# Kernel optimization log

Hardware: AMD Instinct MI355X
Metric: run time of the kernel (lower is better)

The kernel has to match this reference:

```python
import jax, jax.numpy as jnp
import numpy as np

EPS = 1e-5

def layer_norm(x, gamma, beta):
    mu = jnp.mean(x, axis=-1, keepdims=True)
    var = jnp.mean(jnp.square(x - mu), axis=-1, keepdims=True)
    return (x - mu) * jax.lax.rsqrt(var + EPS) * gamma + beta

def reverse_sigmoid(x):
    # torch version clamps value to [0.001, 0.999] with a detached offset ->
    # straight-through: clipped value, identity gradient into the logit.
    y = x + jax.lax.stop_gradient(jnp.clip(x, 0.001, 0.999) - x)
    return jnp.log(y) - jnp.log1p(-y)

def setup_inputs() -> dict:
    key = jax.random.key(0)
    ks = jax.random.split(key, 8)
    N, D, A, F8, FD = 32768, 1024, 256, 8, 64
    inp = {
        "unary_term": jax.random.normal(ks[0], (N, D), jnp.float32),
        "pair_term": jax.random.normal(ks[1], (N, D), jnp.float32),
        "auxiliary_term": jax.random.normal(ks[2], (N, A), jnp.float32),
        "auxiliary_gating_weight": jax.random.uniform(ks[3], (N,), jnp.float32),
        # self.w params: LayerNorm(2D) + Linear(2D, FD)
        "ln_gamma": jnp.ones((2 * D,), jnp.float32),
        "ln_beta": jnp.zeros((2 * D,), jnp.float32),
        "W": jax.random.normal(ks[4], (2 * D, FD), jnp.float32) * 0.02,
        "b": jnp.zeros((FD,), jnp.float32),
        # self.w_aux params: LayerNorm(A) + Linear(A, 8)
        "ln_aux_gamma": jnp.ones((A,), jnp.float32),
        "ln_aux_beta": jnp.zeros((A,), jnp.float32),
        "W_aux": jax.random.normal(ks[5], (A, F8), jnp.float32) * 0.02,
        "b_aux": jnp.zeros((F8,), jnp.float32),
        # use_auxiliary_gate_weight=True -> both init to 0.33
        "gate_weight": jnp.array(0.33, jnp.float32),
        "aux_gate_weight": jnp.array(0.33, jnp.float32),
    }
    return inp

def reference(unary_term, pair_term, auxiliary_term, auxiliary_gating_weight,
              ln_gamma, ln_beta, W, b, ln_aux_gamma, ln_aux_beta, W_aux, b_aux,
              gate_weight, aux_gate_weight):
    # paired_feats = relu(cat([unary, pair], 1))
    paired = jax.nn.relu(jnp.concatenate([unary_term, pair_term], axis=1))  # [N, 2D]
    # gate = sigmoid(Linear(relu(LN(paired))))
    gate = jax.nn.sigmoid(jax.nn.relu(layer_norm(paired, ln_gamma, ln_beta)) @ W + b)  # [N, FD]
    aux_gate = jax.nn.sigmoid(jax.nn.relu(layer_norm(auxiliary_term, ln_aux_gamma, ln_aux_beta)) @ W_aux + b_aux)  # [N, 8]
    gate = jnp.mean(gate, axis=1)        # [N]
    aux_gate = jnp.mean(aux_gate, axis=1)  # [N]
    logit = gate_weight * reverse_sigmoid(gate) + aux_gate_weight * reverse_sigmoid(aux_gate)
    g = jax.nn.sigmoid(logit) * auxiliary_gating_weight  # use_auxiliary_gate_weight=True
    output = pair_term * g[:, None]
    return (output, g)
```

## Files before the change

kernel.cpp:

```cpp
#include <hip/hip_runtime.h>
#include <math.h>


#define EPS_LN 1e-5f

typedef __attribute__((ext_vector_type(8))) short short8;
typedef __attribute__((ext_vector_type(4))) float f32x4;

__device__ __forceinline__ unsigned short f2bf(float f) {
  unsigned int u = __float_as_uint(f);
  u += 0x7FFFu + ((u >> 16) & 1u);
  return (unsigned short)(u >> 16);
}

__device__ __forceinline__ float wsum64(float v) {
  v += __shfl_xor(v, 32);
  v += __shfl_xor(v, 16);
  v += __shfl_xor(v, 8);
  v += __shfl_xor(v, 4);
  v += __shfl_xor(v, 2);
  v += __shfl_xor(v, 1);
  return v;
}

__device__ __forceinline__ float sigmoidf_(float x) {
  return 1.0f / (1.0f + __expf(-x));
}

__device__ __forceinline__ float rsigf(float x) {
  float y = fminf(fmaxf(x, 0.001f), 0.999f);
  return logf(y) - log1pf(-y);
}

__device__ __forceinline__ ushort4 norm_pack(float4 x, float4 g, float4 b,
                                             float mu, float rstd) {
  ushort4 o;
  o.x = f2bf(fmaxf((x.x - mu) * rstd * g.x + b.x, 0.f));
  o.y = f2bf(fmaxf((x.y - mu) * rstd * g.y + b.y, 0.f));
  o.z = f2bf(fmaxf((x.z - mu) * rstd * g.z + b.z, 0.f));
  o.w = f2bf(fmaxf((x.w - mu) * rstd * g.w + b.w, 0.f));
  return o;
}

__global__ void prep_wfrag(const float* __restrict__ W,
                           unsigned short* __restrict__ wfrag) {
  const int lane = threadIdx.x;
  const int b = blockIdx.x;
  const int ntile = b >> 6;
  const int kb = b & 63;
  const int f = (ntile << 4) + (lane & 15);
  const int kbase = (kb << 5) + ((lane >> 4) << 3);
  unsigned short tmp[8];
#pragma unroll
  for (int j = 0; j < 8; ++j) tmp[j] = f2bf(W[(size_t)(kbase + j) * 64 + f]);
  ushort4* dst = reinterpret_cast<ushort4*>(wfrag + (((size_t)b * 64 + lane) << 3));
  dst[0] = make_ushort4(tmp[0], tmp[1], tmp[2], tmp[3]);
  dst[1] = make_ushort4(tmp[4], tmp[5], tmp[6], tmp[7]);
}

__global__ void __launch_bounds__(256, 2) fused_main(
    const float* __restrict__ unary, const float* __restrict__ pair,
    const float* __restrict__ aux, const float* __restrict__ auxw,
    const float* __restrict__ ln_g, const float* __restrict__ ln_b,
    const float* __restrict__ b_lin,
    const float* __restrict__ ln_ag, const float* __restrict__ ln_ab,
    const float* __restrict__ W_aux, const float* __restrict__ b_aux,
    const float* __restrict__ gw, const float* __restrict__ agw,
    const unsigned short* __restrict__ wfrag,
    float* __restrict__ out, float* __restrict__ out_g) {
  __shared__ unsigned short act_lds[16 * 2048];

  const int tid = threadIdx.x;
  const int w = tid >> 6;
  const int lane = tid & 63;
  const int base = blockIdx.x << 4;

  float auxg0 = 0.f, auxg1 = 0.f, auxg2 = 0.f, auxg3 = 0.f;

#pragma unroll
  for (int i = 0; i < 4; ++i) {
    const int rl = (w << 2) + i;
    const int row = base + rl;
    const int sw = rl & 7;

    const float4* u4 = reinterpret_cast<const float4*>(unary + (size_t)row * 1024);
    const float4* p4 = reinterpret_cast<const float4*>(pair + (size_t)row * 1024);
    float4 uv[4], pv[4];
#pragma unroll
    for (int j = 0; j < 4; ++j) {
      uv[j] = u4[lane + 64 * j];
      pv[j] = p4[lane + 64 * j];
    }
    float s = 0.f, sq = 0.f;
#pragma unroll
    for (int j = 0; j < 4; ++j) {
      uv[j].x = fmaxf(uv[j].x, 0.f); uv[j].y = fmaxf(uv[j].y, 0.f);
      uv[j].z = fmaxf(uv[j].z, 0.f); uv[j].w = fmaxf(uv[j].w, 0.f);
      pv[j].x = fmaxf(pv[j].x, 0.f); pv[j].y = fmaxf(pv[j].y, 0.f);
      pv[j].z = fmaxf(pv[j].z, 0.f); pv[j].w = fmaxf(pv[j].w, 0.f);
      s += uv[j].x + uv[j].y + uv[j].z + uv[j].w;
      s += pv[j].x + pv[j].y + pv[j].z + pv[j].w;
      sq += uv[j].x * uv[j].x + uv[j].y * uv[j].y + uv[j].z * uv[j].z + uv[j].w * uv[j].w;
      sq += pv[j].x * pv[j].x + pv[j].y * pv[j].y + pv[j].z * pv[j].z + pv[j].w * pv[j].w;
    }
    s = wsum64(s);
    sq = wsum64(sq);
    const float mu = s * (1.f / 2048.f);
    const float rstd = rsqrtf(sq * (1.f / 2048.f) - mu * mu + EPS_LN);

    const float4* g4 = reinterpret_cast<const float4*>(ln_g);
    const float4* bb4 = reinterpret_cast<const float4*>(ln_b);
#pragma unroll
    for (int j = 0; j < 4; ++j) {
      const int idx = lane + 64 * j;
      const int off = (lane & 1) << 2;
      ushort4 o = norm_pack(uv[j], g4[idx], bb4[idx], mu, rstd);
      int addr = (rl << 11) + ((((idx >> 1)) ^ sw) << 3) + off;
      *reinterpret_cast<ushort4*>(&act_lds[addr]) = o;
      ushort4 o2 = norm_pack(pv[j], g4[256 + idx], bb4[256 + idx], mu, rstd);
      int addr2 = (rl << 11) + (((128 + (idx >> 1)) ^ sw) << 3) + off;
      *reinterpret_cast<ushort4*>(&act_lds[addr2]) = o2;
    }

    const float4 av = reinterpret_cast<const float4*>(aux + (size_t)row * 256)[lane];
    float as = av.x + av.y + av.z + av.w;
    float asq = av.x * av.x + av.y * av.y + av.z * av.z + av.w * av.w;
    as = wsum64(as);
    asq = wsum64(asq);
    const float amu = as * (1.f / 256.f);
    const float arstd = rsqrtf(asq * (1.f / 256.f) - amu * amu + EPS_LN);
    const float4 ag = reinterpret_cast<const float4*>(ln_ag)[lane];
    const float4 ab = reinterpret_cast<const float4*>(ln_ab)[lane];
    float aa[4];
    aa[0] = fmaxf((av.x - amu) * arstd * ag.x + ab.x, 0.f);
    aa[1] = fmaxf((av.y - amu) * arstd * ag.y + ab.y, 0.f);
    aa[2] = fmaxf((av.z - amu) * arstd * ag.z + ab.z, 0.f);
    aa[3] = fmaxf((av.w - amu) * arstd * ag.w + ab.w, 0.f);
    float pf[8];
#pragma unroll
    for (int f = 0; f < 8; ++f) pf[f] = 0.f;
#pragma unroll
    for (int t = 0; t < 4; ++t) {
      const float4* wr = reinterpret_cast<const float4*>(W_aux + (((size_t)lane << 2) + t) * 8);
      float4 wa = wr[0], wb = wr[1];
      pf[0] += aa[t] * wa.x; pf[1] += aa[t] * wa.y;
      pf[2] += aa[t] * wa.z; pf[3] += aa[t] * wa.w;
      pf[4] += aa[t] * wb.x; pf[5] += aa[t] * wb.y;
      pf[6] += aa[t] * wb.z; pf[7] += aa[t] * wb.w;
    }
    float ss = 0.f;
#pragma unroll
    for (int f = 0; f < 8; ++f) {
      float v = wsum64(pf[f]);
      ss += sigmoidf_(v + b_aux[f]);
    }
    const float agv = ss * (1.f / 8.f);
    if (i == 0) auxg0 = agv;
    else if (i == 1) auxg1 = agv;
    else if (i == 2) auxg2 = agv;
    else auxg3 = agv;
  }

  __syncthreads();

  f32x4 acc = {0.f, 0.f, 0.f, 0.f};
  const int arow = lane & 15;
  const int quad = lane >> 4;
  const int abase = arow << 11;
  const int asw = arow & 7;
  const unsigned short* wbase = wfrag + ((size_t)(w << 6) << 9);
#pragma unroll 8
  for (int kb = 0; kb < 64; ++kb) {
    const int c = (kb << 2) + quad;
    const short8 afrag =
        *reinterpret_cast<const short8*>(&act_lds[abase + ((c ^ asw) << 3)]);
    const short8 bfrag =
        *reinterpret_cast<const short8*>(wbase + ((size_t)kb << 9) + (lane << 3));
    acc = __builtin_amdgcn_mfma_f32_16x16x32_bf16(afrag, bfrag, acc, 0, 0, 0);
  }

  const float bl = b_lin[(w << 4) + arow];
  float sred[4];
#pragma unroll
  for (int i = 0; i < 4; ++i) {
    float v = sigmoidf_(acc[i] + bl);
    v += __shfl_xor(v, 1);
    v += __shfl_xor(v, 2);
    v += __shfl_xor(v, 4);
    v += __shfl_xor(v, 8);
    sred[i] = v;
  }

  __syncthreads();
  float* gate_part = reinterpret_cast<float*>(act_lds);
  if (arow == 0) {
#pragma unroll
    for (int i = 0; i < 4; ++i)
      gate_part[(w << 4) + (quad << 2) + i] = sred[i];
  }
  __syncthreads();

  const float gwt = gw[0];
  const float agwt = agw[0];
#pragma unroll
  for (int i = 0; i < 4; ++i) {
    const int rl = (w << 2) + i;
    const int row = base + rl;
    const float gsum = gate_part[rl] + gate_part[16 + rl] +
                       gate_part[32 + rl] + gate_part[48 + rl];
    const float gate = gsum * (1.f / 64.f);
    const float auxg = (i == 0) ? auxg0 : (i == 1) ? auxg1 : (i == 2) ? auxg2 : auxg3;
    const float logit = gwt * rsigf(gate) + agwt * rsigf(auxg);
    const float g = sigmoidf_(logit) * auxw[row];

    const float4* p4 = reinterpret_cast<const float4*>(pair + (size_t)row * 1024);
    float4* o4 = reinterpret_cast<float4*>(out + (size_t)row * 1024);
#pragma unroll
    for (int j = 0; j < 4; ++j) {
      float4 pv = p4[lane + 64 * j];
      pv.x *= g; pv.y *= g; pv.z *= g; pv.w *= g;
      o4[lane + 64 * j] = pv;
    }
    if (lane == 0) out_g[row] = g;
  }
}

extern "C" void kernel_launch(void* const* d_in, const int* in_sizes, int n_in,
                              void* d_out, int out_size, void* d_ws, size_t ws_size,
                              hipStream_t stream) {
  const float* unary = (const float*)d_in[0];
  const float* pair  = (const float*)d_in[1];
  const float* aux   = (const float*)d_in[2];
  const float* auxw  = (const float*)d_in[3];
  const float* ln_g  = (const float*)d_in[4];
  const float* ln_b  = (const float*)d_in[5];
  const float* W     = (const float*)d_in[6];
  const float* b     = (const float*)d_in[7];
  const float* ln_ag = (const float*)d_in[8];
  const float* ln_ab = (const float*)d_in[9];
  const float* W_aux = (const float*)d_in[10];
  const float* b_aux = (const float*)d_in[11];
  const float* gw    = (const float*)d_in[12];
  const float* agw   = (const float*)d_in[13];

  const int N = in_sizes[3];
  unsigned short* wfrag = (unsigned short*)d_ws;
  float* out = (float*)d_out;
  float* out_g = out + (size_t)N * 1024;

  prep_wfrag<<<256, 64, 0, stream>>>(W, wfrag);
  fused_main<<<N / 16, 256, 0, stream>>>(unary, pair, aux, auxw, ln_g, ln_b, b,
                                         ln_ag, ln_ab, W_aux, b_aux, gw, agw,
                                         wfrag, out, out_g);
}
```

Baseline: 480.9 us.

## Halve rows per block, raise occupancy, and move aux linear to MFMA

Each block now handles 8 rows instead of 16, which halves LDS use per block and lets launch bounds ask for 4 blocks per CU instead of 2, so more loads can be in flight on this memory-bound kernel. The auxiliary LayerNorm+Linear now writes bf16 activations to LDS and does its matmul with MFMA, using W_aux repacked by the prep kernel. This replaces the scalar FMA loop and its eight 64-lane shuffle reductions. The four LayerNorm reductions are merged into one shuffle loop. In exchange, half of each 16-row MFMA tile is wasted, and the aux path drops to bf16 precision.

```diff
diff --git a/kernel.cpp b/kernel.cpp
--- a/kernel.cpp
+++ b/kernel.cpp
@@ -11,16 +11,6 @@
   unsigned int u = __float_as_uint(f);
   u += 0x7FFFu + ((u >> 16) & 1u);
   return (unsigned short)(u >> 16);
-}
-
-__device__ __forceinline__ float wsum64(float v) {
-  v += __shfl_xor(v, 32);
-  v += __shfl_xor(v, 16);
-  v += __shfl_xor(v, 8);
-  v += __shfl_xor(v, 4);
-  v += __shfl_xor(v, 2);
-  v += __shfl_xor(v, 1);
-  return v;
 }
 
 __device__ __forceinline__ float sigmoidf_(float x) {
@@ -43,45 +33,59 @@
 }
 
 __global__ void prep_wfrag(const float* __restrict__ W,
+                           const float* __restrict__ W_aux,
                            unsigned short* __restrict__ wfrag) {
   const int lane = threadIdx.x;
   const int b = blockIdx.x;
-  const int ntile = b >> 6;
-  const int kb = b & 63;
-  const int f = (ntile << 4) + (lane & 15);
-  const int kbase = (kb << 5) + ((lane >> 4) << 3);
   unsigned short tmp[8];
-#pragma unroll
-  for (int j = 0; j < 8; ++j) tmp[j] = f2bf(W[(size_t)(kbase + j) * 64 + f]);
-  ushort4* dst = reinterpret_cast<ushort4*>(wfrag + (((size_t)b * 64 + lane) << 3));
-  dst[0] = make_ushort4(tmp[0], tmp[1], tmp[2], tmp[3]);
-  dst[1] = make_ushort4(tmp[4], tmp[5], tmp[6], tmp[7]);
-}
-
-__global__ void __launch_bounds__(256, 2) fused_main(
+  if (b < 256) {
+    const int ntile = b >> 6;
+    const int kb = b & 63;
+    const int f = (ntile << 4) + (lane & 15);
+    const int kbase = (kb << 5) + ((lane >> 4) << 3);
+#pragma unroll
+    for (int j = 0; j < 8; ++j) tmp[j] = f2bf(W[(size_t)(kbase + j) * 64 + f]);
+    ushort4* dst = reinterpret_cast<ushort4*>(wfrag + (((size_t)b * 64 + lane) << 3));
+    dst[0] = make_ushort4(tmp[0], tmp[1], tmp[2], tmp[3]);
+    dst[1] = make_ushort4(tmp[4], tmp[5], tmp[6], tmp[7]);
+  } else {
+    const int kb = b - 256;
+    const int f = lane & 15;
+    const int kbase = (kb << 5) + ((lane >> 4) << 3);
+#pragma unroll
+    for (int j = 0; j < 8; ++j)
+      tmp[j] = (f < 8) ? f2bf(W_aux[(size_t)(kbase + j) * 8 + f]) : (unsigned short)0;
+    ushort4* dst = reinterpret_cast<ushort4*>(
+        wfrag + 131072 + (((size_t)kb * 64 + lane) << 3));
+    dst[0] = make_ushort4(tmp[0], tmp[1], tmp[2], tmp[3]);
+    dst[1] = make_ushort4(tmp[4], tmp[5], tmp[6], tmp[7]);
+  }
+}
+
+__global__ void __launch_bounds__(256, 4) fused_main(
     const float* __restrict__ unary, const float* __restrict__ pair,
     const float* __restrict__ aux, const float* __restrict__ auxw,
     const float* __restrict__ ln_g, const float* __restrict__ ln_b,
     const float* __restrict__ b_lin,
     const float* __restrict__ ln_ag, const float* __restrict__ ln_ab,
-    const float* __restrict__ W_aux, const float* __restrict__ b_aux,
+    const float* __restrict__ b_aux,
     const float* __restrict__ gw, const float* __restrict__ agw,
     const unsigned short* __restrict__ wfrag,
     float* __restrict__ out, float* __restrict__ out_g) {
-  __shared__ unsigned short act_lds[16 * 2048];
+  __shared__ unsigned short act_lds[8 * 2048];
+  __shared__ unsigned short aux_lds[8 * 256];
+  __shared__ float gate_part[4 * 8];
+  __shared__ float auxg_lds[8];
 
   const int tid = threadIdx.x;
   const int w = tid >> 6;
   const int lane = tid & 63;
-  const int base = blockIdx.x << 4;
-
-  float auxg0 = 0.f, auxg1 = 0.f, auxg2 = 0.f, auxg3 = 0.f;
-
-#pragma unroll
-  for (int i = 0; i < 4; ++i) {
-    const int rl = (w << 2) + i;
+  const int base = blockIdx.x << 3;
+
+#pragma unroll
+  for (int i = 0; i < 2; ++i) {
+    const int rl = (w << 1) + i;
     const int row = base + rl;
-    const int sw = rl & 7;
 
     const float4* u4 = reinterpret_cast<const float4*>(unary + (size_t)row * 1024);
     const float4* p4 = reinterpret_cast<const float4*>(pair + (size_t)row * 1024);
@@ -91,6 +95,8 @@
       uv[j] = u4[lane + 64 * j];
       pv[j] = p4[lane + 64 * j];
     }
+    const float4 av = reinterpret_cast<const float4*>(aux + (size_t)row * 256)[lane];
+
     float s = 0.f, sq = 0.f;
 #pragma unroll
     for (int j = 0; j < 4; ++j) {
@@ -103,10 +109,20 @@
       sq += uv[j].x * uv[j].x + uv[j].y * uv[j].y + uv[j].z * uv[j].z + uv[j].w * uv[j].w;
       sq += pv[j].x * pv[j].x + pv[j].y * pv[j].y + pv[j].z * pv[j].z + pv[j].w * pv[j].w;
     }
-    s = wsum64(s);
-    sq = wsum64(sq);
+    float as = av.x + av.y + av.z + av.w;
+    float asq = av.x * av.x + av.y * av.y + av.z * av.z + av.w * av.w;
+
+#pragma unroll
+    for (int d = 32; d; d >>= 1) {
+      s += __shfl_xor(s, d);
+      sq += __shfl_xor(sq, d);
+      as += __shfl_xor(as, d);
+      asq += __shfl_xor(asq, d);
+    }
     const float mu = s * (1.f / 2048.f);
     const float rstd = rsqrtf(sq * (1.f / 2048.f) - mu * mu + EPS_LN);
+    const float amu = as * (1.f / 256.f);
+    const float arstd = rsqrtf(asq * (1.f / 256.f) - amu * amu + EPS_LN);
 
     const float4* g4 = reinterpret_cast<const float4*>(ln_g);
     const float4* bb4 = reinterpret_cast<const float4*>(ln_b);
@@ -115,71 +131,50 @@
       const int idx = lane + 64 * j;
       const int off = (lane & 1) << 2;
       ushort4 o = norm_pack(uv[j], g4[idx], bb4[idx], mu, rstd);
-      int addr = (rl << 11) + ((((idx >> 1)) ^ sw) << 3) + off;
+      int addr = (rl << 11) + ((((idx >> 1)) ^ rl) << 3) + off;
       *reinterpret_cast<ushort4*>(&act_lds[addr]) = o;
       ushort4 o2 = norm_pack(pv[j], g4[256 + idx], bb4[256 + idx], mu, rstd);
-      int addr2 = (rl << 11) + (((128 + (idx >> 1)) ^ sw) << 3) + off;
+      int addr2 = (rl << 11) + (((128 + (idx >> 1)) ^ rl) << 3) + off;
       *reinterpret_cast<ushort4*>(&act_lds[addr2]) = o2;
     }
-
-    const float4 av = reinterpret_cast<const float4*>(aux + (size_t)row * 256)[lane];
-    float as = av.x + av.y + av.z + av.w;
-    float asq = av.x * av.x + av.y * av.y + av.z * av.z + av.w * av.w;
-    as = wsum64(as);
-    asq = wsum64(asq);
-    const float amu = as * (1.f / 256.f);
-    const float arstd = rsqrtf(asq * (1.f / 256.f) - amu * amu + EPS_LN);
-    const float4 ag = reinterpret_cast<const float4*>(ln_ag)[lane];
-    const float4 ab = reinterpret_cast<const float4*>(ln_ab)[lane];
-    float aa[4];
-    aa[0] = fmaxf((av.x - amu) * arstd * ag.x + ab.x, 0.f);
-    aa[1] = fmaxf((av.y - amu) * arstd * ag.y + ab.y, 0.f);
-    aa[2] = fmaxf((av.z - amu) * arstd * ag.z + ab.z, 0.f);
-    aa[3] = fmaxf((av.w - amu) * arstd * ag.w + ab.w, 0.f);
-    float pf[8];
-#pragma unroll
-    for (int f = 0; f < 8; ++f) pf[f] = 0.f;
-#pragma unroll
-    for (int t = 0; t < 4; ++t) {
-      const float4* wr = reinterpret_cast<const float4*>(W_aux + (((size_t)lane << 2) + t) * 8);
-      float4 wa = wr[0], wb = wr[1];
-      pf[0] += aa[t] * wa.x; pf[1] += aa[t] * wa.y;
-      pf[2] += aa[t] * wa.z; pf[3] += aa[t] * wa.w;
-      pf[4] += aa[t] * wb.x; pf[5] += aa[t] * wb.y;
-      pf[6] += aa[t] * wb.z; pf[7] += aa[t] * wb.w;
-    }
-    float ss = 0.f;
-#pragma unroll
-    for (int f = 0; f < 8; ++f) {
-      float v = wsum64(pf[f]);
-      ss += sigmoidf_(v + b_aux[f]);
-    }
-    const float agv = ss * (1.f / 8.f);
-    if (i == 0) auxg0 = agv;
-    else if (i == 1) auxg1 = agv;
-    else if (i == 2) auxg2 = agv;
-    else auxg3 = agv;
+    {
+      const float4 ag = reinterpret_cast<const float4*>(ln_ag)[lane];
+      const float4 ab = reinterpret_cast<const float4*>(ln_ab)[lane];
+      ushort4 ao = norm_pack(av, ag, ab, amu, arstd);
+      int addr = (rl << 8) + ((((lane >> 1)) ^ rl) << 3) + ((lane & 1) << 2);
+      *reinterpret_cast<ushort4*>(&aux_lds[addr]) = ao;
+    }
   }
 
   __syncthreads();
 
   f32x4 acc = {0.f, 0.f, 0.f, 0.f};
-  const int arow = lane & 15;
+  const int arow = lane & 7;
   const int quad = lane >> 4;
-  const int abase = arow << 11;
-  const int asw = arow & 7;
-  const unsigned short* wbase = wfrag + ((size_t)(w << 6) << 9);
+  const unsigned short* wbase = wfrag + (((size_t)(w << 6)) << 9);
 #pragma unroll 8
   for (int kb = 0; kb < 64; ++kb) {
-    const int c = (kb << 2) + quad;
-    const short8 afrag =
-        *reinterpret_cast<const short8*>(&act_lds[abase + ((c ^ asw) << 3)]);
-    const short8 bfrag =
-        *reinterpret_cast<const short8*>(wbase + ((size_t)kb << 9) + (lane << 3));
+    const short8 afrag = *reinterpret_cast<const short8*>(
+        &act_lds[(arow << 11) + ((((kb << 2) + quad) ^ arow) << 3)]);
+    const short8 bfrag = *reinterpret_cast<const short8*>(
+        wbase + ((size_t)kb << 9) + (lane << 3));
     acc = __builtin_amdgcn_mfma_f32_16x16x32_bf16(afrag, bfrag, acc, 0, 0, 0);
   }
-
-  const float bl = b_lin[(w << 4) + arow];
+  f32x4 aacc = {0.f, 0.f, 0.f, 0.f};
+  if (w == 0) {
+    const unsigned short* abase = wfrag + 131072;
+#pragma unroll
+    for (int kb = 0; kb < 8; ++kb) {
+      const short8 afrag = *reinterpret_cast<const short8*>(
+          &aux_lds[(arow << 8) + ((((kb << 2) + quad) ^ arow) << 3)]);
+      const short8 bfrag = *reinterpret_cast<const short8*>(
+          abase + ((size_t)kb << 9) + (lane << 3));
+      aacc = __builtin_amdgcn_mfma_f32_16x16x32_bf16(afrag, bfrag, aacc, 0, 0, 0);
+    }
+  }
+
+  const int col = lane & 15;
+  const float bl = b_lin[(w << 4) + col];
   float sred[4];
 #pragma unroll
   for (int i = 0; i < 4; ++i) {
@@ -190,26 +185,34 @@
     v += __shfl_xor(v, 8);
     sred[i] = v;
   }
-
-  __syncthreads();
-  float* gate_part = reinterpret_cast<float*>(act_lds);
-  if (arow == 0) {
+  if (col == 0 && quad < 2) {
 #pragma unroll
     for (int i = 0; i < 4; ++i)
-      gate_part[(w << 4) + (quad << 2) + i] = sred[i];
+      gate_part[(w << 3) + (quad << 2) + i] = sred[i];
+  }
+  if (w == 0) {
+    const float ba = b_aux[col & 7];
+#pragma unroll
+    for (int i = 0; i < 4; ++i) {
+      float v = (col < 8) ? sigmoidf_(aacc[i] + ba) : 0.f;
+      v += __shfl_xor(v, 1);
+      v += __shfl_xor(v, 2);
+      v += __shfl_xor(v, 4);
+      v += __shfl_xor(v, 8);
+      if (col == 0 && quad < 2) auxg_lds[(quad << 2) + i] = v * 0.125f;
+    }
   }
   __syncthreads();
 
   const float gwt = gw[0];
   const float agwt = agw[0];
 #pragma unroll
-  for (int i = 0; i < 4; ++i) {
-    const int rl = (w << 2) + i;
+  for (int i = 0; i < 2; ++i) {
+    const int rl = (w << 1) + i;
     const int row = base + rl;
-    const float gsum = gate_part[rl] + gate_part[16 + rl] +
-                       gate_part[32 + rl] + gate_part[48 + rl];
-    const float gate = gsum * (1.f / 64.f);
-    const float auxg = (i == 0) ? auxg0 : (i == 1) ? auxg1 : (i == 2) ? auxg2 : auxg3;
+    const float gate = (gate_part[rl] + gate_part[8 + rl] +
+                        gate_part[16 + rl] + gate_part[24 + rl]) * (1.f / 64.f);
+    const float auxg = auxg_lds[rl];
     const float logit = gwt * rsigf(gate) + agwt * rsigf(auxg);
     const float g = sigmoidf_(logit) * auxw[row];
 
@@ -248,8 +251,8 @@
   float* out = (float*)d_out;
   float* out_g = out + (size_t)N * 1024;
 
-  prep_wfrag<<<256, 64, 0, stream>>>(W, wfrag);
-  fused_main<<<N / 16, 256, 0, stream>>>(unary, pair, aux, auxw, ln_g, ln_b, b,
-                                         ln_ag, ln_ab, W_aux, b_aux, gw, agw,
-                                         wfrag, out, out_g);
-}
+  prep_wfrag<<<264, 64, 0, stream>>>(W, W_aux, wfrag);
+  fused_main<<<N / 8, 256, 0, stream>>>(unary, pair, aux, auxw, ln_g, ln_b, b,
+                                        ln_ag, ln_ab, b_aux, gw, agw,
+                                        wfrag, out, out_g);
+}
```

Measured after the change: 493.0 us. +2.5%, slower.
